# Kernel optimization log

Hardware: AMD Instinct MI355X
Metric: run time of the kernel (lower is better)

## Reference

```python
import jax, jax.numpy as jnp
import numpy as np

K, Q, DIM = 64, 128, 1024
TF_W, DE_W, FFT_W = 1.0, 0.8, 0.6  # opt.TF_weight / DE_weight / FFT_weight


def setup_inputs() -> dict:
    key = jax.random.key(0)
    ks = jax.random.split(key, 9)
    def feats(k):
        return jax.random.normal(k, (K, Q, DIM), dtype=jnp.float32)
    def protos(k):
        return jax.random.normal(k, (K, DIM), dtype=jnp.float32)
    def var(k):
        # positive variances, bounded away from zero
        return jax.random.uniform(k, (K,), dtype=jnp.float32) + 0.5
    return {
        "TFq_output": feats(ks[0]), "TFs_proto": protos(ks[1]), "TF_variance": var(ks[2]),
        "DEq_output": feats(ks[3]), "DEs_proto": protos(ks[4]), "DE_variance": var(ks[5]),
        "FFTq_output": feats(ks[6]), "FFTs_proto": protos(ks[7]), "FFT_variance": var(ks[8]),
    }


def _mah_dist(xq, proto, variance):
    # ||x - p||^2 / var via expansion: avoids materializing (num, protonum, dim)
    x2 = jnp.sum(xq * xq, axis=1, keepdims=True)            # (num, 1)
    p2 = jnp.sum(proto * proto, axis=1)[None, :]            # (1, protonum)
    xp = xq @ proto.T                                       # (num, protonum)
    return (x2 - 2.0 * xp + p2) / variance[None, :]


def _modality(xq, proto, variance, w):
    logits = -_mah_dist(xq, proto, variance)
    pred = w * jax.nn.softmax(logits, axis=1)
    mahloss = -(w * jax.nn.log_softmax(logits, axis=1))
    return pred, mahloss


def reference(TFq_output, TFs_proto, TF_variance,
              DEq_output, DEs_proto, DE_variance,
              FFTq_output, FFTs_proto, FFT_variance):
    k, q, _ = TFq_output.shape
    y = jnp.repeat(jnp.arange(k), q)                         # (k*q,)

    tf_pred, tf_loss = _modality(TFq_output.reshape(k * q, -1), TFs_proto, TF_variance, TF_W)
    de_pred, de_loss = _modality(DEq_output.reshape(k * q, -1), DEs_proto, DE_variance, DE_W)
    fft_pred, fft_loss = _modality(FFTq_output.reshape(k * q, -1), FFTs_proto, FFT_variance, FFT_W)

    fusion_loss = tf_loss + de_loss + fft_loss               # (k*q, k)
    loss = jnp.take_along_axis(fusion_loss, y[:, None], axis=1).squeeze(-1).mean()

    pred_mah = tf_pred + de_pred + fft_pred
    pred = jnp.argmax(pred_mah, axis=1)
    acc = (pred == y).astype(jnp.float32).mean()
    return (loss, acc)
```

## Files before the change

### kernel.cpp

```cpp
#include <hip/hip_runtime.h>


typedef _Float16 half8 __attribute__((ext_vector_type(8)));
typedef float    floatx4 __attribute__((ext_vector_type(4)));

#define NCLS   64
#define QPC    128
#define DIM    1024
#define NROWS  (NCLS * QPC)
#define NRT    (NROWS / 16)
#define UW2    132

#define OFF_W      0
#define W_BYTES    (3 * NCLS * DIM * 2)
#define OFF_P2     W_BYTES
#define OFF_PRED   397312
#define PRED_BYTES (3 * NROWS * NCLS * 4)
#define OFF_LP     (OFF_PRED + PRED_BYTES)
#define OFF_CP     (OFF_LP + 3 * NRT * 4)
#define WS_NEED    (OFF_CP + NRT * 4)

__device__ __forceinline__ void dma4(const float* g, float* l) {
    __builtin_amdgcn_global_load_lds(
        (const __attribute__((address_space(1))) void*)g,
        (__attribute__((address_space(3))) void*)l,
        4, 0, 0);
}

__global__ __launch_bounds__(64) void prep_protos(
    const float* __restrict__ Ptf, const float* __restrict__ Pde,
    const float* __restrict__ Pff, _Float16* __restrict__ W,
    float* __restrict__ p2)
{
    const int m    = blockIdx.x >> 5;
    const int kcg  = blockIdx.x & 31;
    const int lane = threadIdx.x;
    const int l15  = lane & 15;
    const int quad = lane >> 4;
    const float* __restrict__ P = (m == 0) ? Ptf : (m == 1) ? Pde : Pff;

    #pragma unroll
    for (int t = 0; t < 4; ++t) {
        const float* src = P + (size_t)(t * 16 + l15) * DIM + kcg * 32 + quad * 8;
        const float4 b0 = *reinterpret_cast<const float4*>(src);
        const float4 b1 = *reinterpret_cast<const float4*>(src + 4);
        half8 h;
        h[0] = (_Float16)b0.x; h[1] = (_Float16)b0.y;
        h[2] = (_Float16)b0.z; h[3] = (_Float16)b0.w;
        h[4] = (_Float16)b1.x; h[5] = (_Float16)b1.y;
        h[6] = (_Float16)b1.z; h[7] = (_Float16)b1.w;
        *reinterpret_cast<half8*>(W + ((size_t)(m * 32 + kcg) * 4 + t) * 512 + lane * 8) = h;

        float s = b0.x*b0.x + b0.y*b0.y + b0.z*b0.z + b0.w*b0.w
                + b1.x*b1.x + b1.y*b1.y + b1.z*b1.z + b1.w*b1.w;
        s += __shfl_xor(s, 16);
        s += __shfl_xor(s, 32);
        if (quad == 0) atomicAdd(&p2[m * 64 + t * 16 + l15], s);
    }
}

__global__ __launch_bounds__(256, 8) void fusion_main(
    const float* __restrict__ Xtf, const float* __restrict__ Xde,
    const float* __restrict__ Xff,
    const float* __restrict__ Vtf, const float* __restrict__ Vde,
    const float* __restrict__ Vff,
    const _Float16* __restrict__ W, const float* __restrict__ p2g,
    float* __restrict__ predOut,
    float* __restrict__ lossPart)
{
    __shared__ float buf[2][16 * UW2];
    __shared__ float x2s[16];
    __shared__ float mxW[4][16];
    __shared__ float sW[4][16];
    __shared__ float lossW[4];

    const int tid  = threadIdx.x;
    const int w    = tid >> 6;
    const int lane = tid & 63;
    const int l15  = lane & 15;
    const int quad = lane >> 4;
    const int b    = blockIdx.x;
    const int m    = b >> 9;
    const int rt   = b & 511;
    const int rowBase = rt * 16;

    const float* __restrict__ X = (m == 0) ? Xtf : (m == 1) ? Xde : Xff;
    const float* __restrict__ V = (m == 0) ? Vtf : (m == 1) ? Vde : Vff;
    const float  wgt = (m == 0) ? 1.0f : (m == 1) ? 0.8f : 0.6f;

    const float* gb = X + (size_t)(rowBase + w * 4) * DIM + lane;

    floatx4 d = (floatx4){0.f, 0.f, 0.f, 0.f};
    float x2p = 0.0f;

    #pragma unroll
    for (int r4 = 0; r4 < 4; ++r4) {
        dma4(gb + (size_t)r4 * DIM,      &buf[0][(w * 4 + r4) * UW2]);
        dma4(gb + (size_t)r4 * DIM + 64, &buf[0][(w * 4 + r4) * UW2 + 64]);
    }

    #pragma unroll
    for (int c = 0; c < 8; ++c) {
        __syncthreads();
        if (c < 7) {
            const float* g1 = gb + (c + 1) * 128;
            float* lb = &buf[(c + 1) & 1][0];
            #pragma unroll
            for (int r4 = 0; r4 < 4; ++r4) {
                dma4(g1 + (size_t)r4 * DIM,      lb + (w * 4 + r4) * UW2);
                dma4(g1 + (size_t)r4 * DIM + 64, lb + (w * 4 + r4) * UW2 + 64);
            }
        }
        const float* tb = &buf[c & 1][0];
        #pragma unroll
        for (int kc = 0; kc < 4; ++kc) {
            const int off = l15 * UW2 + kc * 32 + quad * 8;
            const float4 a0 = *reinterpret_cast<const float4*>(tb + off);
            const float4 a1 = *reinterpret_cast<const float4*>(tb + off + 4);
            const int kcg = c * 4 + kc;
            const half8 bf = *reinterpret_cast<const half8*>(
                W + ((size_t)(m * 32 + kcg) * 4 + w) * 512 + lane * 8);

            if (w == 0)
                x2p += a0.x*a0.x + a0.y*a0.y + a0.z*a0.z + a0.w*a0.w
                     + a1.x*a1.x + a1.y*a1.y + a1.z*a1.z + a1.w*a1.w;

            half8 af;
            af[0] = (_Float16)a0.x; af[1] = (_Float16)a0.y;
            af[2] = (_Float16)a0.z; af[3] = (_Float16)a0.w;
            af[4] = (_Float16)a1.x; af[5] = (_Float16)a1.y;
            af[6] = (_Float16)a1.z; af[7] = (_Float16)a1.w;

            d = __builtin_amdgcn_mfma_f32_16x16x32_f16(af, bf, d, 0, 0, 0);
        }
    }

    if (w == 0) {
        x2p += __shfl_xor(x2p, 16);
        x2p += __shfl_xor(x2p, 32);
        if (quad == 0) x2s[l15] = x2p;
    }
    __syncthreads();

    const int col = w * 16 + l15;
    const float vc  = V[col];
    const float p2c = p2g[m * 64 + col];
    float lg[4];
    #pragma unroll
    for (int r = 0; r < 4; ++r)
        lg[r] = (2.0f * d[r] - x2s[quad * 4 + r] - p2c) / vc;

    #pragma unroll
    for (int r = 0; r < 4; ++r) {
        float mx = lg[r];
        #pragma unroll
        for (int dl = 1; dl <= 8; dl <<= 1) mx = fmaxf(mx, __shfl_xor(mx, dl));
        if (l15 == 0) mxW[w][quad * 4 + r] = mx;
    }
    __syncthreads();

    float gmx[4];
    #pragma unroll
    for (int r = 0; r < 4; ++r) {
        const int row = quad * 4 + r;
        gmx[r] = fmaxf(fmaxf(mxW[0][row], mxW[1][row]),
                       fmaxf(mxW[2][row], mxW[3][row]));
        float s = expf(lg[r] - gmx[r]);
        #pragma unroll
        for (int dl = 1; dl <= 8; dl <<= 1) s += __shfl_xor(s, dl);
        if (l15 == 0) sW[w][quad * 4 + r] = s;
    }
    __syncthreads();

    const int y = rowBase >> 7;
    float lossAcc = 0.0f;
    #pragma unroll
    for (int r = 0; r < 4; ++r) {
        const int row = quad * 4 + r;
        const float lse = gmx[r] + logf(sW[0][row] + sW[1][row]
                                      + sW[2][row] + sW[3][row]);
        if (col == y) lossAcc += wgt * (lse - lg[r]);
        predOut[((size_t)m * NROWS + rowBase + row) * 64 + col] =
            wgt * expf(lg[r] - lse);
    }
    #pragma unroll
    for (int dl = 1; dl <= 32; dl <<= 1) lossAcc += __shfl_xor(lossAcc, dl);
    if (lane == 0) lossW[w] = lossAcc;
    __syncthreads();
    if (tid == 0) lossPart[b] = lossW[0] + lossW[1] + lossW[2] + lossW[3];
}

__global__ __launch_bounds__(256) void finalize1(
    const float* __restrict__ pred, float* __restrict__ cntPart)
{
    const int rt   = blockIdx.x;
    const int tid  = threadIdx.x;
    const int v    = tid >> 6;
    const int lane = tid & 63;

    float cnt = 0.0f;
    #pragma unroll
    for (int r4 = 0; r4 < 4; ++r4) {
        const int R = rt * 16 + v * 4 + r4;
        const int y = R >> 7;
        float p = pred[(size_t)R * 64 + lane]
                + pred[((size_t)NROWS + R) * 64 + lane]
                + pred[((size_t)2 * NROWS + R) * 64 + lane];
        float bv = p; int bc = lane;
        #pragma unroll
        for (int dl = 1; dl <= 32; dl <<= 1) {
            const float ov = __shfl_xor(bv, dl);
            const int   oc = __shfl_xor(bc, dl);
            if (ov > bv || (ov == bv && oc < bc)) { bv = ov; bc = oc; }
        }
        if (lane == 0 && bc == y) cnt += 1.0f;
    }
    #pragma unroll
    for (int dl = 1; dl <= 32; dl <<= 1) cnt += __shfl_xor(cnt, dl);
    __shared__ float sc[4];
    if (lane == 0) sc[v] = cnt;
    __syncthreads();
    if (tid == 0) cntPart[rt] = sc[0] + sc[1] + sc[2] + sc[3];
}

__global__ __launch_bounds__(256) void finalize2(
    const float* __restrict__ lossPart, const float* __restrict__ cntPart,
    float* __restrict__ out)
{
    const int tid  = threadIdx.x;
    const int lane = tid & 63;
    const int v    = tid >> 6;
    float l = 0.0f, c = 0.0f;
    for (int i = tid; i < 3 * NRT; i += 256) l += lossPart[i];
    for (int i = tid; i < NRT; i += 256)     c += cntPart[i];
    #pragma unroll
    for (int dl = 1; dl <= 32; dl <<= 1) {
        l += __shfl_xor(l, dl);
        c += __shfl_xor(c, dl);
    }
    __shared__ float sl[4], sc[4];
    if (lane == 0) { sl[v] = l; sc[v] = c; }
    __syncthreads();
    if (tid == 0) {
        out[0] = (sl[0] + sl[1] + sl[2] + sl[3]) * (1.0f / NROWS);
        out[1] = (sc[0] + sc[1] + sc[2] + sc[3]) * (1.0f / NROWS);
    }
}

#define NWAVES 12
#define KSPLIT 4
#define KSLICE (DIM / KSPLIT)
#define NITER  (KSLICE / 32)
#define DSTRIDE 17
#define PSTRIDE 65

__global__ __launch_bounds__(NWAVES * 64) void fusion_loss_fallback(
    const float* __restrict__ Xtf, const float* __restrict__ Ptf, const float* __restrict__ Vtf,
    const float* __restrict__ Xde, const float* __restrict__ Pde, const float* __restrict__ Vde,
    const float* __restrict__ Xff, const float* __restrict__ Pff, const float* __restrict__ Vff,
    float* __restrict__ out)
{
    __shared__ float dpart[NWAVES][64 * DSTRIDE];
    __shared__ float x2part[NWAVES][16];
    __shared__ float p2part[NWAVES][64];
    __shared__ float predL[16 * PSTRIDE];
    __shared__ float lossL;

    const int tid  = threadIdx.x;
    const int wave = tid >> 6;
    const int lane = tid & 63;
    const int l15  = lane & 15;
    const int quad = lane >> 4;
    const int m    = wave >> 2;
    const int kq   = wave & 3;
    const int rowBase = blockIdx.x * 16;

    for (int i = tid; i < 16 * PSTRIDE; i += NWAVES * 64) predL[i] = 0.0f;
    if (tid == 0) lossL = 0.0f;

    const float* __restrict__ X = (m == 0) ? Xtf : (m == 1) ? Xde : Xff;
    const float* __restrict__ P = (m == 0) ? Ptf : (m == 1) ? Pde : Pff;
    const float* __restrict__ V = (m == 0) ? Vtf : (m == 1) ? Vde : Vff;
    const float  w = (m == 0) ? 1.0f : (m == 1) ? 0.8f : 0.6f;

    floatx4 d[4];
    #pragma unroll
    for (int t = 0; t < 4; ++t) d[t] = (floatx4){0.f, 0.f, 0.f, 0.f};
    float x2p    = 0.0f;
    float p2p[4] = {0.f, 0.f, 0.f, 0.f};

    const float* xrow = X + (size_t)(rowBase + l15) * DIM + kq * KSLICE + quad * 8;
    const float* prow[4];
    #pragma unroll
    for (int t = 0; t < 4; ++t)
        prow[t] = P + (size_t)(t * 16 + l15) * DIM + kq * KSLICE + quad * 8;

    #pragma unroll 2
    for (int kc = 0; kc < NITER; ++kc) {
        const int ko = kc * 32;
        const float4 a0 = *reinterpret_cast<const float4*>(xrow + ko);
        const float4 a1 = *reinterpret_cast<const float4*>(xrow + ko + 4);
        float4 b0[4], b1[4];
        #pragma unroll
        for (int t = 0; t < 4; ++t) {
            b0[t] = *reinterpret_cast<const float4*>(prow[t] + ko);
            b1[t] = *reinterpret_cast<const float4*>(prow[t] + ko + 4);
        }
        x2p += a0.x*a0.x + a0.y*a0.y + a0.z*a0.z + a0.w*a0.w
             + a1.x*a1.x + a1.y*a1.y + a1.z*a1.z + a1.w*a1.w;
        half8 af;
        af[0] = (_Float16)a0.x; af[1] = (_Float16)a0.y;
        af[2] = (_Float16)a0.z; af[3] = (_Float16)a0.w;
        af[4] = (_Float16)a1.x; af[5] = (_Float16)a1.y;
        af[6] = (_Float16)a1.z; af[7] = (_Float16)a1.w;
        #pragma unroll
        for (int t = 0; t < 4; ++t) {
            p2p[t] += b0[t].x*b0[t].x + b0[t].y*b0[t].y + b0[t].z*b0[t].z + b0[t].w*b0[t].w
                    + b1[t].x*b1[t].x + b1[t].y*b1[t].y + b1[t].z*b1[t].z + b1[t].w*b1[t].w;
            half8 bf;
            bf[0] = (_Float16)b0[t].x; bf[1] = (_Float16)b0[t].y;
            bf[2] = (_Float16)b0[t].z; bf[3] = (_Float16)b0[t].w;
            bf[4] = (_Float16)b1[t].x; bf[5] = (_Float16)b1[t].y;
            bf[6] = (_Float16)b1[t].z; bf[7] = (_Float16)b1[t].w;
            d[t] = __builtin_amdgcn_mfma_f32_16x16x32_f16(af, bf, d[t], 0, 0, 0);
        }
    }

    x2p += __shfl_xor(x2p, 16);
    x2p += __shfl_xor(x2p, 32);
    #pragma unroll
    for (int t = 0; t < 4; ++t) {
        p2p[t] += __shfl_xor(p2p[t], 16);
        p2p[t] += __shfl_xor(p2p[t], 32);
    }
    {
        float* dp = &dpart[wave][lane * DSTRIDE];
        #pragma unroll
        for (int t = 0; t < 4; ++t)
            *reinterpret_cast<float4*>(dp + t * 4) =
                make_float4(d[t][0], d[t][1], d[t][2], d[t][3]);
        if (quad == 0) {
            x2part[wave][l15] = x2p;
            #pragma unroll
            for (int t = 0; t < 4; ++t) p2part[wave][t * 16 + l15] = p2p[t];
        }
    }
    __syncthreads();

    const int y = rowBase >> 7;

    if (kq == 0) {
        floatx4 dsum[4];
        #pragma unroll
        for (int t = 0; t < 4; ++t) dsum[t] = (floatx4){0.f, 0.f, 0.f, 0.f};
        float x2r[4] = {0.f, 0.f, 0.f, 0.f};
        float p2c[4] = {0.f, 0.f, 0.f, 0.f};
        #pragma unroll
        for (int k2 = 0; k2 < KSPLIT; ++k2) {
            const int wv = m * 4 + k2;
            const float* src = &dpart[wv][lane * DSTRIDE];
            #pragma unroll
            for (int t = 0; t < 4; ++t) {
                const float4 vv = *reinterpret_cast<const float4*>(src + t * 4);
                dsum[t][0] += vv.x; dsum[t][1] += vv.y; dsum[t][2] += vv.z; dsum[t][3] += vv.w;
            }
            #pragma unroll
            for (int r = 0; r < 4; ++r) x2r[r] += x2part[wv][quad * 4 + r];
            #pragma unroll
            for (int t = 0; t < 4; ++t) p2c[t] += p2part[wv][t * 16 + l15];
        }
        float vc[4];
        #pragma unroll
        for (int t = 0; t < 4; ++t) vc[t] = V[t * 16 + l15];

        float lossAcc = 0.0f;
        #pragma unroll
        for (int r = 0; r < 4; ++r) {
            float lg[4];
            #pragma unroll
            for (int t = 0; t < 4; ++t)
                lg[t] = (2.0f * dsum[t][r] - x2r[r] - p2c[t]) / vc[t];
            float mx = fmaxf(fmaxf(lg[0], lg[1]), fmaxf(lg[2], lg[3]));
            #pragma unroll
            for (int dl = 1; dl <= 8; dl <<= 1) mx = fmaxf(mx, __shfl_xor(mx, dl));
            float s = expf(lg[0] - mx) + expf(lg[1] - mx)
                    + expf(lg[2] - mx) + expf(lg[3] - mx);
            #pragma unroll
            for (int dl = 1; dl <= 8; dl <<= 1) s += __shfl_xor(s, dl);
            const float lse = mx + logf(s);
            const int row = quad * 4 + r;
            #pragma unroll
            for (int t = 0; t < 4; ++t) {
                const int colc = t * 16 + l15;
                if (colc == y) lossAcc += w * (lse - lg[t]);
                atomicAdd(&predL[row * PSTRIDE + colc], w * expf(lg[t] - lse));
            }
        }
        #pragma unroll
        for (int dl = 1; dl <= 32; dl <<= 1) lossAcc += __shfl_xor(lossAcc, dl);
        if (lane == 0) atomicAdd(&lossL, lossAcc);
    }
    __syncthreads();

    if (wave == 0) {
        float cnt = 0.0f;
        #pragma unroll 1
        for (int r = 0; r < 16; ++r) {
            float bv = predL[r * PSTRIDE + lane];
            int   bc = lane;
            #pragma unroll
            for (int dl = 1; dl <= 32; dl <<= 1) {
                const float ov = __shfl_xor(bv, dl);
                const int   oc = __shfl_xor(bc, dl);
                if (ov > bv || (ov == bv && oc < bc)) { bv = ov; bc = oc; }
            }
            if (lane == 0 && bc == y) cnt += 1.0f;
        }
        if (lane == 0) {
            atomicAdd(&out[0], lossL * (1.0f / NROWS));
            atomicAdd(&out[1], cnt * (1.0f / NROWS));
        }
    }
}

extern "C" void kernel_launch(void* const* d_in, const int* in_sizes, int n_in,
                              void* d_out, int out_size, void* d_ws, size_t ws_size,
                              hipStream_t stream) {
    const float* Xtf = (const float*)d_in[0];
    const float* Ptf = (const float*)d_in[1];
    const float* Vtf = (const float*)d_in[2];
    const float* Xde = (const float*)d_in[3];
    const float* Pde = (const float*)d_in[4];
    const float* Vde = (const float*)d_in[5];
    const float* Xff = (const float*)d_in[6];
    const float* Pff = (const float*)d_in[7];
    const float* Vff = (const float*)d_in[8];
    float* out = (float*)d_out;

    if (ws_size >= (size_t)WS_NEED) {
        char* ws = (char*)d_ws;
        _Float16* W     = (_Float16*)(ws + OFF_W);
        float*    p2    = (float*)(ws + OFF_P2);
        float*    pred  = (float*)(ws + OFF_PRED);
        float*    lossP = (float*)(ws + OFF_LP);
        float*    cntP  = (float*)(ws + OFF_CP);

        hipMemsetAsync(p2, 0, 3 * NCLS * sizeof(float), stream);
        prep_protos<<<dim3(96), dim3(64), 0, stream>>>(Ptf, Pde, Pff, W, p2);
        fusion_main<<<dim3(3 * NRT), dim3(256), 0, stream>>>(
            Xtf, Xde, Xff, Vtf, Vde, Vff, W, p2, pred, lossP);
        finalize1<<<dim3(NRT), dim3(256), 0, stream>>>(pred, cntP);
        finalize2<<<dim3(1), dim3(256), 0, stream>>>(lossP, cntP, out);
    } else {
        hipMemsetAsync(out, 0, 2 * sizeof(float), stream);
        fusion_loss_fallback<<<dim3(NROWS / 16), dim3(NWAVES * 64), 0, stream>>>(
            Xtf, Ptf, Vtf, Xde, Pde, Vde, Xff, Pff, Vff, out);
    }
}
```

Baseline: 156.2 us.

## Fuse three modalities and argmax into one block, drop pred buffer

Merges the per-modality main kernel and the accuracy finalize kernel into one 768-thread block that handles all three modalities for a 16-row tile. Per-modality probabilities are summed in shared memory and reduced to an argmax on chip, so the 6 MB pred buffer is no longer written and read back and one launch disappears. The LDS double-buffered async staging of X is replaced by direct per-lane float4 global loads, which may lose coalescing and latency hiding, and each wave now loads X redundantly (4 waves per modality read the same rows).

```diff
diff --git a/kernel.cpp b/kernel.cpp
--- a/kernel.cpp
+++ b/kernel.cpp
@@ -9,23 +9,13 @@
 #define DIM    1024
 #define NROWS  (NCLS * QPC)
 #define NRT    (NROWS / 16)
-#define UW2    132
 
 #define OFF_W      0
 #define W_BYTES    (3 * NCLS * DIM * 2)
 #define OFF_P2     W_BYTES
-#define OFF_PRED   397312
-#define PRED_BYTES (3 * NROWS * NCLS * 4)
-#define OFF_LP     (OFF_PRED + PRED_BYTES)
-#define OFF_CP     (OFF_LP + 3 * NRT * 4)
+#define OFF_LP     (OFF_P2 + 3 * NCLS * 4)
+#define OFF_CP     (OFF_LP + NRT * 4)
 #define WS_NEED    (OFF_CP + NRT * 4)
-
-__device__ __forceinline__ void dma4(const float* g, float* l) {
-    __builtin_amdgcn_global_load_lds(
-        (const __attribute__((address_space(1))) void*)g,
-        (__attribute__((address_space(3))) void*)l,
-        4, 0, 0);
-}
 
 __global__ __launch_bounds__(64) void prep_protos(
     const float* __restrict__ Ptf, const float* __restrict__ Pde,
@@ -59,103 +49,81 @@
     }
 }
 
-__global__ __launch_bounds__(256, 8) void fusion_main(
+__global__ __launch_bounds__(768, 6) void fusion_all(
     const float* __restrict__ Xtf, const float* __restrict__ Xde,
     const float* __restrict__ Xff,
     const float* __restrict__ Vtf, const float* __restrict__ Vde,
     const float* __restrict__ Vff,
     const _Float16* __restrict__ W, const float* __restrict__ p2g,
-    float* __restrict__ predOut,
-    float* __restrict__ lossPart)
+    float* __restrict__ lossPart,
+    float* __restrict__ cntPart)
 {
-    __shared__ float buf[2][16 * UW2];
-    __shared__ float x2s[16];
-    __shared__ float mxW[4][16];
-    __shared__ float sW[4][16];
-    __shared__ float lossW[4];
+    __shared__ float x2s[3][16];
+    __shared__ float mxW[3][4][16];
+    __shared__ float sW[3][4][16];
+    __shared__ float predS[3][16][66];
+    __shared__ float lossW[12];
+    __shared__ float cntW[4];
 
     const int tid  = threadIdx.x;
     const int w    = tid >> 6;
     const int lane = tid & 63;
     const int l15  = lane & 15;
     const int quad = lane >> 4;
-    const int b    = blockIdx.x;
-    const int m    = b >> 9;
-    const int rt   = b & 511;
-    const int rowBase = rt * 16;
+    const int m    = w >> 2;
+    const int cq   = w & 3;
+    const int rowBase = blockIdx.x * 16;
 
     const float* __restrict__ X = (m == 0) ? Xtf : (m == 1) ? Xde : Xff;
     const float* __restrict__ V = (m == 0) ? Vtf : (m == 1) ? Vde : Vff;
     const float  wgt = (m == 0) ? 1.0f : (m == 1) ? 0.8f : 0.6f;
 
-    const float* gb = X + (size_t)(rowBase + w * 4) * DIM + lane;
+    const float* __restrict__ xr = X + (size_t)(rowBase + l15) * DIM + quad * 8;
+    const _Float16* __restrict__ wb = W + ((size_t)(m * 32) * 4 + cq) * 512 + lane * 8;
 
     floatx4 d = (floatx4){0.f, 0.f, 0.f, 0.f};
     float x2p = 0.0f;
 
-    #pragma unroll
-    for (int r4 = 0; r4 < 4; ++r4) {
-        dma4(gb + (size_t)r4 * DIM,      &buf[0][(w * 4 + r4) * UW2]);
-        dma4(gb + (size_t)r4 * DIM + 64, &buf[0][(w * 4 + r4) * UW2 + 64]);
-    }
-
-    #pragma unroll
-    for (int c = 0; c < 8; ++c) {
-        __syncthreads();
-        if (c < 7) {
-            const float* g1 = gb + (c + 1) * 128;
-            float* lb = &buf[(c + 1) & 1][0];
-            #pragma unroll
-            for (int r4 = 0; r4 < 4; ++r4) {
-                dma4(g1 + (size_t)r4 * DIM,      lb + (w * 4 + r4) * UW2);
-                dma4(g1 + (size_t)r4 * DIM + 64, lb + (w * 4 + r4) * UW2 + 64);
-            }
-        }
-        const float* tb = &buf[c & 1][0];
-        #pragma unroll
-        for (int kc = 0; kc < 4; ++kc) {
-            const int off = l15 * UW2 + kc * 32 + quad * 8;
-            const float4 a0 = *reinterpret_cast<const float4*>(tb + off);
-            const float4 a1 = *reinterpret_cast<const float4*>(tb + off + 4);
-            const int kcg = c * 4 + kc;
-            const half8 bf = *reinterpret_cast<const half8*>(
-                W + ((size_t)(m * 32 + kcg) * 4 + w) * 512 + lane * 8);
-
-            if (w == 0)
-                x2p += a0.x*a0.x + a0.y*a0.y + a0.z*a0.z + a0.w*a0.w
-                     + a1.x*a1.x + a1.y*a1.y + a1.z*a1.z + a1.w*a1.w;
-
-            half8 af;
-            af[0] = (_Float16)a0.x; af[1] = (_Float16)a0.y;
-            af[2] = (_Float16)a0.z; af[3] = (_Float16)a0.w;
-            af[4] = (_Float16)a1.x; af[5] = (_Float16)a1.y;
-            af[6] = (_Float16)a1.z; af[7] = (_Float16)a1.w;
-
-            d = __builtin_amdgcn_mfma_f32_16x16x32_f16(af, bf, d, 0, 0, 0);
-        }
-    }
-
-    if (w == 0) {
+    #pragma unroll 2
+    for (int kc = 0; kc < 32; ++kc) {
+        const float4 a0 = *reinterpret_cast<const float4*>(xr + kc * 32);
+        const float4 a1 = *reinterpret_cast<const float4*>(xr + kc * 32 + 4);
+        const half8 bf = *reinterpret_cast<const half8*>(wb + (size_t)kc * 2048);
+
+        if (cq == 0)
+            x2p += a0.x*a0.x + a0.y*a0.y + a0.z*a0.z + a0.w*a0.w
+                 + a1.x*a1.x + a1.y*a1.y + a1.z*a1.z + a1.w*a1.w;
+
+        half8 af;
+        af[0] = (_Float16)a0.x; af[1] = (_Float16)a0.y;
+        af[2] = (_Float16)a0.z; af[3] = (_Float16)a0.w;
+        af[4] = (_Float16)a1.x; af[5] = (_Float16)a1.y;
+        af[6] = (_Float16)a1.z; af[7] = (_Float16)a1.w;
+
+        d = __builtin_amdgcn_mfma_f32_16x16x32_f16(af, bf, d, 0, 0, 0);
+    }
+
+    if (cq == 0) {
         x2p += __shfl_xor(x2p, 16);
         x2p += __shfl_xor(x2p, 32);
-        if (quad == 0) x2s[l15] = x2p;
-    }
-    __syncthreads();
-
-    const int col = w * 16 + l15;
+        if (quad == 0) x2s[m][l15] = x2p;
+    }
+    __syncthreads();
+
+    const int col = cq * 16 + l15;
     const float vc  = V[col];
     const float p2c = p2g[m * 64 + col];
     float lg[4];
     #pragma unroll
     for (int r = 0; r < 4; ++r)
-        lg[r] = (2.0f * d[r] - x2s[quad * 4 + r] - p2c) / vc;
+        lg[r] = (2.0f * d[r] - x2s[m][quad * 4 + r] - p2c) / vc;
 
     #pragma unroll
     for (int r = 0; r < 4; ++r) {
         float mx = lg[r];
         #pragma unroll
         for (int dl = 1; dl <= 8; dl <<= 1) mx = fmaxf(mx, __shfl_xor(mx, dl));
-        if (l15 == 0) mxW[w][quad * 4 + r] = mx;
+        if (l15 == 0) mxW[m][cq][quad * 4 + r] = mx;
     }
     __syncthreads();
 
@@ -163,12 +131,12 @@
     #pragma unroll
     for (int r = 0; r < 4; ++r) {
         const int row = quad * 4 + r;
-        gmx[r] = fmaxf(fmaxf(mxW[0][row], mxW[1][row]),
-                       fmaxf(mxW[2][row], mxW[3][row]));
+        gmx[r] = fmaxf(fmaxf(mxW[m][0][row], mxW[m][1][row]),
+                       fmaxf(mxW[m][2][row], mxW[m][3][row]));
         float s = expf(lg[r] - gmx[r]);
         #pragma unroll
         for (int dl = 1; dl <= 8; dl <<= 1) s += __shfl_xor(s, dl);
-        if (l15 == 0) sW[w][quad * 4 + r] = s;
+        if (l15 == 0) sW[m][cq][quad * 4 + r] = s;
     }
     __syncthreads();
 
@@ -177,50 +145,43 @@
     #pragma unroll
     for (int r = 0; r < 4; ++r) {
         const int row = quad * 4 + r;
-        const float lse = gmx[r] + logf(sW[0][row] + sW[1][row]
-                                      + sW[2][row] + sW[3][row]);
+        const float lse = gmx[r] + logf(sW[m][0][row] + sW[m][1][row]
+                                      + sW[m][2][row] + sW[m][3][row]);
         if (col == y) lossAcc += wgt * (lse - lg[r]);
-        predOut[((size_t)m * NROWS + rowBase + row) * 64 + col] =
-            wgt * expf(lg[r] - lse);
+        predS[m][row][col] = wgt * expf(lg[r] - lse);
     }
     #pragma unroll
     for (int dl = 1; dl <= 32; dl <<= 1) lossAcc += __shfl_xor(lossAcc, dl);
     if (lane == 0) lossW[w] = lossAcc;
     __syncthreads();
-    if (tid == 0) lossPart[b] = lossW[0] + lossW[1] + lossW[2] + lossW[3];
-}
-
-__global__ __launch_bounds__(256) void finalize1(
-    const float* __restrict__ pred, float* __restrict__ cntPart)
-{
-    const int rt   = blockIdx.x;
-    const int tid  = threadIdx.x;
-    const int v    = tid >> 6;
-    const int lane = tid & 63;
-
-    float cnt = 0.0f;
-    #pragma unroll
-    for (int r4 = 0; r4 < 4; ++r4) {
-        const int R = rt * 16 + v * 4 + r4;
-        const int y = R >> 7;
-        float p = pred[(size_t)R * 64 + lane]
-                + pred[((size_t)NROWS + R) * 64 + lane]
-                + pred[((size_t)2 * NROWS + R) * 64 + lane];
-        float bv = p; int bc = lane;
-        #pragma unroll
-        for (int dl = 1; dl <= 32; dl <<= 1) {
-            const float ov = __shfl_xor(bv, dl);
-            const int   oc = __shfl_xor(bc, dl);
-            if (ov > bv || (ov == bv && oc < bc)) { bv = ov; bc = oc; }
-        }
-        if (lane == 0 && bc == y) cnt += 1.0f;
-    }
-    #pragma unroll
-    for (int dl = 1; dl <= 32; dl <<= 1) cnt += __shfl_xor(cnt, dl);
-    __shared__ float sc[4];
-    if (lane == 0) sc[v] = cnt;
-    __syncthreads();
-    if (tid == 0) cntPart[rt] = sc[0] + sc[1] + sc[2] + sc[3];
+
+    if (w < 4) {
+        float cnt = 0.0f;
+        #pragma unroll
+        for (int r4 = 0; r4 < 4; ++r4) {
+            const int row = w * 4 + r4;
+            float bv = predS[0][row][lane] + predS[1][row][lane]
+                     + predS[2][row][lane];
+            int bc = lane;
+            #pragma unroll
+            for (int dl = 1; dl <= 32; dl <<= 1) {
+                const float ov = __shfl_xor(bv, dl);
+                const int   oc = __shfl_xor(bc, dl);
+                if (ov > bv || (ov == bv && oc < bc)) { bv = ov; bc = oc; }
+            }
+            if (bc == y) cnt += 1.0f;
+        }
+        if (lane == 0) cntW[w] = cnt;
+    }
+    __syncthreads();
+
+    if (tid == 0) {
+        float L = 0.0f;
+        #pragma unroll
+        for (int i = 0; i < 12; ++i) L += lossW[i];
+        lossPart[blockIdx.x] = L;
+        cntPart[blockIdx.x]  = cntW[0] + cntW[1] + cntW[2] + cntW[3];
+    }
 }
 
 __global__ __launch_bounds__(256) void finalize2(
@@ -231,8 +192,8 @@
     const int lane = tid & 63;
     const int v    = tid >> 6;
     float l = 0.0f, c = 0.0f;
-    for (int i = tid; i < 3 * NRT; i += 256) l += lossPart[i];
-    for (int i = tid; i < NRT; i += 256)     c += cntPart[i];
+    for (int i = tid; i < NRT; i += 256) l += lossPart[i];
+    for (int i = tid; i < NRT; i += 256) c += cntPart[i];
     #pragma unroll
     for (int dl = 1; dl <= 32; dl <<= 1) {
         l += __shfl_xor(l, dl);
@@ -441,15 +402,13 @@
         char* ws = (char*)d_ws;
         _Float16* W     = (_Float16*)(ws + OFF_W);
         float*    p2    = (float*)(ws + OFF_P2);
-        float*    pred  = (float*)(ws + OFF_PRED);
         float*    lossP = (float*)(ws + OFF_LP);
         float*    cntP  = (float*)(ws + OFF_CP);
 
         hipMemsetAsync(p2, 0, 3 * NCLS * sizeof(float), stream);
         prep_protos<<<dim3(96), dim3(64), 0, stream>>>(Ptf, Pde, Pff, W, p2);
-        fusion_main<<<dim3(3 * NRT), dim3(256), 0, stream>>>(
-            Xtf, Xde, Xff, Vtf, Vde, Vff, W, p2, pred, lossP);
-        finalize1<<<dim3(NRT), dim3(256), 0, stream>>>(pred, cntP);
+        fusion_all<<<dim3(NRT), dim3(768), 0, stream>>>(
+            Xtf, Xde, Xff, Vtf, Vde, Vff, W, p2, lossP, cntP);
         finalize2<<<dim3(1), dim3(256), 0, stream>>>(lossP, cntP, out);
     } else {
         hipMemsetAsync(out, 0, 2 * sizeof(float), stream);
```

Result: slower. 176.6 us (+13.1%).

## Load full 16-row tile via 16-byte LDS DMA with swizzle; drop p2 memset

Applied to the files above, without the earlier changes.

The main kernel now loads the whole 16x1024 fp32 row tile into LDS up front, using 16-byte global_load_lds transfers with an XOR swizzle. This replaces the double-buffered 4-byte DMA loop and its per-chunk barriers. The cost is 64KB of LDS per block, which limits occupancy to about 2 blocks per CU and removes load/compute overlap inside a block. prep_protos is also restructured to reduce per-row norms through LDS instead of atomics, which removes the memset launch.

```diff
diff --git a/kernel.cpp b/kernel.cpp
--- a/kernel.cpp
+++ b/kernel.cpp
@@ -9,7 +9,6 @@
 #define DIM    1024
 #define NROWS  (NCLS * QPC)
 #define NRT    (NROWS / 16)
-#define UW2    132
 
 #define OFF_W      0
 #define W_BYTES    (3 * NCLS * DIM * 2)
@@ -20,30 +19,36 @@
 #define OFF_CP     (OFF_LP + 3 * NRT * 4)
 #define WS_NEED    (OFF_CP + NRT * 4)
 
-__device__ __forceinline__ void dma4(const float* g, float* l) {
+__device__ __forceinline__ void dma16(const float* g, float* l) {
     __builtin_amdgcn_global_load_lds(
         (const __attribute__((address_space(1))) void*)g,
         (__attribute__((address_space(3))) void*)l,
-        4, 0, 0);
-}
-
-__global__ __launch_bounds__(64) void prep_protos(
+        16, 0, 0);
+}
+
+__global__ __launch_bounds__(256) void prep_protos(
     const float* __restrict__ Ptf, const float* __restrict__ Pde,
     const float* __restrict__ Pff, _Float16* __restrict__ W,
     float* __restrict__ p2)
 {
-    const int m    = blockIdx.x >> 5;
-    const int kcg  = blockIdx.x & 31;
-    const int lane = threadIdx.x;
+    __shared__ float p2w[4][16];
+
+    const int m    = blockIdx.x >> 2;
+    const int t    = blockIdx.x & 3;
+    const int tid  = threadIdx.x;
+    const int v    = tid >> 6;
+    const int lane = tid & 63;
     const int l15  = lane & 15;
     const int quad = lane >> 4;
     const float* __restrict__ P = (m == 0) ? Ptf : (m == 1) ? Pde : Pff;
 
-    #pragma unroll
-    for (int t = 0; t < 4; ++t) {
-        const float* src = P + (size_t)(t * 16 + l15) * DIM + kcg * 32 + quad * 8;
-        const float4 b0 = *reinterpret_cast<const float4*>(src);
-        const float4 b1 = *reinterpret_cast<const float4*>(src + 4);
+    const float* src = P + (size_t)(t * 16 + l15) * DIM + quad * 8;
+    float s = 0.0f;
+    #pragma unroll
+    for (int i = 0; i < 8; ++i) {
+        const int kcg = v * 8 + i;
+        const float4 b0 = *reinterpret_cast<const float4*>(src + kcg * 32);
+        const float4 b1 = *reinterpret_cast<const float4*>(src + kcg * 32 + 4);
         half8 h;
         h[0] = (_Float16)b0.x; h[1] = (_Float16)b0.y;
         h[2] = (_Float16)b0.z; h[3] = (_Float16)b0.w;
@@ -51,15 +56,19 @@
         h[6] = (_Float16)b1.z; h[7] = (_Float16)b1.w;
         *reinterpret_cast<half8*>(W + ((size_t)(m * 32 + kcg) * 4 + t) * 512 + lane * 8) = h;
 
-        float s = b0.x*b0.x + b0.y*b0.y + b0.z*b0.z + b0.w*b0.w
-                + b1.x*b1.x + b1.y*b1.y + b1.z*b1.z + b1.w*b1.w;
-        s += __shfl_xor(s, 16);
-        s += __shfl_xor(s, 32);
-        if (quad == 0) atomicAdd(&p2[m * 64 + t * 16 + l15], s);
-    }
-}
-
-__global__ __launch_bounds__(256, 8) void fusion_main(
+        s += b0.x*b0.x + b0.y*b0.y + b0.z*b0.z + b0.w*b0.w
+           + b1.x*b1.x + b1.y*b1.y + b1.z*b1.z + b1.w*b1.w;
+    }
+    s += __shfl_xor(s, 16);
+    s += __shfl_xor(s, 32);
+    if (quad == 0) p2w[v][l15] = s;
+    __syncthreads();
+    if (v == 0 && quad == 0)
+        p2[m * 64 + t * 16 + l15] = p2w[0][l15] + p2w[1][l15]
+                                  + p2w[2][l15] + p2w[3][l15];
+}
+
+__global__ __launch_bounds__(256, 2) void fusion_m(
     const float* __restrict__ Xtf, const float* __restrict__ Xde,
     const float* __restrict__ Xff,
     const float* __restrict__ Vtf, const float* __restrict__ Vde,
@@ -68,7 +77,7 @@
     float* __restrict__ predOut,
     float* __restrict__ lossPart)
 {
-    __shared__ float buf[2][16 * UW2];
+    __shared__ __align__(16) float tile[16][1024];
     __shared__ float x2s[16];
     __shared__ float mxW[4][16];
     __shared__ float sW[4][16];
@@ -88,51 +97,45 @@
     const float* __restrict__ V = (m == 0) ? Vtf : (m == 1) ? Vde : Vff;
     const float  wgt = (m == 0) ? 1.0f : (m == 1) ? 0.8f : 0.6f;
 
-    const float* gb = X + (size_t)(rowBase + w * 4) * DIM + lane;
+    #pragma unroll
+    for (int j = 0; j < 16; ++j) {
+        const int row = w * 4 + (j >> 2);
+        const int q   = j & 3;
+        const int swz = (row & 7) * 4;
+        const float* g = X + (size_t)(rowBase + row) * DIM
+                       + q * 256 + ((lane * 4) ^ swz);
+        dma16(g, &tile[row][q * 256]);
+    }
+    __syncthreads();
+
+    const _Float16* __restrict__ wb =
+        W + ((size_t)(m * 32) * 4 + w) * 512 + lane * 8;
+    const int sw = (l15 & 7) * 4;
+    const float* tb = &tile[l15][0];
 
     floatx4 d = (floatx4){0.f, 0.f, 0.f, 0.f};
     float x2p = 0.0f;
 
-    #pragma unroll
-    for (int r4 = 0; r4 < 4; ++r4) {
-        dma4(gb + (size_t)r4 * DIM,      &buf[0][(w * 4 + r4) * UW2]);
-        dma4(gb + (size_t)r4 * DIM + 64, &buf[0][(w * 4 + r4) * UW2 + 64]);
-    }
-
-    #pragma unroll
-    for (int c = 0; c < 8; ++c) {
-        __syncthreads();
-        if (c < 7) {
-            const float* g1 = gb + (c + 1) * 128;
-            float* lb = &buf[(c + 1) & 1][0];
-            #pragma unroll
-            for (int r4 = 0; r4 < 4; ++r4) {
-                dma4(g1 + (size_t)r4 * DIM,      lb + (w * 4 + r4) * UW2);
-                dma4(g1 + (size_t)r4 * DIM + 64, lb + (w * 4 + r4) * UW2 + 64);
-            }
-        }
-        const float* tb = &buf[c & 1][0];
-        #pragma unroll
-        for (int kc = 0; kc < 4; ++kc) {
-            const int off = l15 * UW2 + kc * 32 + quad * 8;
-            const float4 a0 = *reinterpret_cast<const float4*>(tb + off);
-            const float4 a1 = *reinterpret_cast<const float4*>(tb + off + 4);
-            const int kcg = c * 4 + kc;
-            const half8 bf = *reinterpret_cast<const half8*>(
-                W + ((size_t)(m * 32 + kcg) * 4 + w) * 512 + lane * 8);
-
-            if (w == 0)
-                x2p += a0.x*a0.x + a0.y*a0.y + a0.z*a0.z + a0.w*a0.w
-                     + a1.x*a1.x + a1.y*a1.y + a1.z*a1.z + a1.w*a1.w;
-
-            half8 af;
-            af[0] = (_Float16)a0.x; af[1] = (_Float16)a0.y;
-            af[2] = (_Float16)a0.z; af[3] = (_Float16)a0.w;
-            af[4] = (_Float16)a1.x; af[5] = (_Float16)a1.y;
-            af[6] = (_Float16)a1.z; af[7] = (_Float16)a1.w;
-
-            d = __builtin_amdgcn_mfma_f32_16x16x32_f16(af, bf, d, 0, 0, 0);
-        }
+    #pragma unroll 8
+    for (int kc = 0; kc < 32; ++kc) {
+        const float4 a0 = *reinterpret_cast<const float4*>(
+            tb + kc * 32 + ((quad * 8) ^ sw));
+        const float4 a1 = *reinterpret_cast<const float4*>(
+            tb + kc * 32 + (((quad * 8) + 4) ^ sw));
+        const half8 bf = *reinterpret_cast<const half8*>(
+            wb + (size_t)kc * 2048);
+
+        if (w == 0)
+            x2p += a0.x*a0.x + a0.y*a0.y + a0.z*a0.z + a0.w*a0.w
+                 + a1.x*a1.x + a1.y*a1.y + a1.z*a1.z + a1.w*a1.w;
+
+        half8 af;
+        af[0] = (_Float16)a0.x; af[1] = (_Float16)a0.y;
+        af[2] = (_Float16)a0.z; af[3] = (_Float16)a0.w;
+        af[4] = (_Float16)a1.x; af[5] = (_Float16)a1.y;
+        af[6] = (_Float16)a1.z; af[7] = (_Float16)a1.w;
+
+        d = __builtin_amdgcn_mfma_f32_16x16x32_f16(af, bf, d, 0, 0, 0);
     }
 
     if (w == 0) {
@@ -445,9 +448,8 @@
         float*    lossP = (float*)(ws + OFF_LP);
         float*    cntP  = (float*)(ws + OFF_CP);
 
-        hipMemsetAsync(p2, 0, 3 * NCLS * sizeof(float), stream);
-        prep_protos<<<dim3(96), dim3(64), 0, stream>>>(Ptf, Pde, Pff, W, p2);
-        fusion_main<<<dim3(3 * NRT), dim3(256), 0, stream>>>(
+        prep_protos<<<dim3(12), dim3(256), 0, stream>>>(Ptf, Pde, Pff, W, p2);
+        fusion_m<<<dim3(3 * NRT), dim3(256), 0, stream>>>(
             Xtf, Xde, Xff, Vtf, Vde, Vff, W, p2, pred, lossP);
         finalize1<<<dim3(NRT), dim3(256), 0, stream>>>(pred, cntP);
         finalize2<<<dim3(1), dim3(256), 0, stream>>>(lossP, cntP, out);
```

Result: slower. 164.2 us (+5.2%).
